# Optimization experiments

Measured on AMD Instinct MI355X. Metric: run time of the kernel, lower is better.

## Reference

```python
import jax, jax.numpy as jnp
import numpy as np

E = 8192       # number of edges
D = 256        # edge feature dim


def setup_inputs() -> dict:
    key = jax.random.key(0)
    ks = jax.random.split(key, 4)
    s = 1.0 / np.sqrt(D)
    return {
        "edge_x": jax.random.normal(ks[0], (E, D), dtype=jnp.float32),
        "W_sim1": jax.random.normal(ks[1], (D, D), dtype=jnp.float32) * s,
        "b_sim1": jnp.zeros((D,), dtype=jnp.float32),
        "W_sim2": jax.random.normal(ks[2], (D, D), dtype=jnp.float32) * s,
        "b_sim2": jnp.zeros((D,), dtype=jnp.float32),
        "W_out": jax.random.normal(ks[3], (3 * D, D), dtype=jnp.float32) * (1.0 / np.sqrt(3 * D)),
        "b_out": jnp.zeros((D,), dtype=jnp.float32),
    }


def reference(edge_x, W_sim1, b_sim1, W_sim2, b_sim2, W_out, b_out):
    # MPModule.forward, 'fully' branch.
    # LinearBlock = Linear + ReLU (assumed).
    e1 = jax.nn.relu(edge_x @ W_sim1 + b_sim1)            # [E, D]
    # (e1.unsqueeze(1) * e1).mean(-1)  ==  (e1 @ e1.T) / D, avoiding [E,E,D]
    sim1 = (e1 @ e1.T) / D                                 # [E, E]
    e2 = jax.nn.relu(edge_x @ W_sim2 + b_sim2)             # [E, D]
    sim2 = (e2 @ e2.T) / D                                 # [E, E]
    # (edge_x * sim.unsqueeze(-1)).sum(1) == sim @ edge_x
    agg1 = sim1 @ edge_x                                   # [E, D]
    agg2 = sim2 @ edge_x                                   # [E, D]
    h = jnp.concatenate([edge_x, agg1, agg2], axis=-1)     # [E, 3D]
    return jax.nn.relu(h @ W_out + b_out)                  # [E, D]
```

## Files before the change

kernel.cpp:

```cpp
#include <hip/hip_runtime.h>
#include <hip/hip_bf16.h>


typedef short bf16x8  __attribute__((ext_vector_type(8)));
typedef short short4v __attribute__((ext_vector_type(4)));
typedef float f32x4   __attribute__((ext_vector_type(4)));

__device__ inline short f2bf(float x) {
    unsigned u = __builtin_bit_cast(unsigned, x);
    return (short)((u + 0x7fffu + ((u >> 16) & 1u)) >> 16);
}
__device__ inline float bf2f(short b) {
    return __builtin_bit_cast(float, (unsigned)((unsigned short)b) << 16);
}
__device__ inline void cp16_async(const char* g, char* l) {
    __builtin_amdgcn_global_load_lds(
        (const __attribute__((address_space(1))) unsigned int*)g,
        (__attribute__((address_space(3))) unsigned int*)l, 16, 0, 0);
}

__device__ __forceinline__ void core128(
    const short* __restrict__ Ap, int lda, const short* __restrict__ Bp, int ldb,
    int kbeg, int kend, int m0, int n0, short* Sf, f32x4 acc[4][4], int t)
{
    const int l = t & 63, lr = l & 15, q = l >> 4;
    const int w = t >> 6, wm = w >> 1, wn = w & 1;
    const int wub = t & ~63;

    auto stage = [&](int buf, int k0) {
        #pragma unroll
        for (int it = 0; it < 4; ++it) {
            int idx = it * 256 + t, r = idx >> 3, s = idx & 7;
            cp16_async((const char*)(Ap + (size_t)(m0 + r) * lda + k0) + s * 16,
                       (char*)(Sf + buf * 16384) + (size_t)(it * 256 + wub) * 16);
        }
        #pragma unroll
        for (int it = 0; it < 4; ++it) {
            int idx = it * 256 + t, r = idx >> 3, s = idx & 7;
            cp16_async((const char*)(Bp + (size_t)(n0 + r) * ldb + k0) + s * 16,
                       (char*)(Sf + buf * 16384 + 8192) + (size_t)(it * 256 + wub) * 16);
        }
    };

    stage(0, kbeg);
    __syncthreads();
    int cur = 0;
    for (int k0 = kbeg; k0 < kend; k0 += 64) {
        if (k0 + 64 < kend) stage(cur ^ 1, k0 + 64);
        const short* As = Sf + cur * 16384;
        const short* Bs = As + 8192;
        #pragma unroll
        for (int ks = 0; ks < 2; ++ks) {
            bf16x8 af[4], bfr[4];
            #pragma unroll
            for (int mt = 0; mt < 4; ++mt) {
                int ar = wm * 64 + mt * 16 + lr;
                af[mt] = *(const bf16x8*)&As[ar * 64 + (((ks*4 + q) ^ (ar & 7)) << 3)];
            }
            #pragma unroll
            for (int nt = 0; nt < 4; ++nt) {
                int br = wn * 64 + nt * 16 + lr;
                bfr[nt] = *(const bf16x8*)&Bs[br * 64 + (((ks*4 + q) ^ (br & 7)) << 3)];
            }
            #pragma unroll
            for (int mt = 0; mt < 4; ++mt)
                #pragma unroll
                for (int nt = 0; nt < 4; ++nt)
                    acc[mt][nt] = __builtin_amdgcn_mfma_f32_16x16x32_bf16(
                        af[mt], bfr[nt], acc[mt][nt], 0, 0, 0);
        }
        __syncthreads();
        cur ^= 1;
    }
}

__global__ __launch_bounds__(256, 1)
void d1_eg(const float* __restrict__ X,
           const float* __restrict__ W1, const float* __restrict__ b1v,
           const float* __restrict__ W2, const float* __restrict__ b2v,
           const float* __restrict__ Wo,
           short* __restrict__ h, short* __restrict__ e1t, short* __restrict__ e2t,
           short* __restrict__ G1t, short* __restrict__ G2t,
           short* __restrict__ Bt4, int* __restrict__ ticket)
{
    const int bx = blockIdx.x, by = blockIdx.y, z = blockIdx.z;
    const int t = threadIdx.x;
    const int l = t & 63, lr = l & 15, q = l >> 4;
    const int w = t >> 6, wm = w >> 1, wn = w & 1;

    if (bx == 0 && by == 0 && z == 0 && t == 0) { ticket[0] = 0; ticket[1] = 0; }

    __shared__ __attribute__((aligned(16))) short S[32768];

    if (z == 2 && by == 0) {
        short (*tile)[33] = (short(*)[33])S;
        const int tx = t & 31, ty = t >> 5;
        const int kx = bx >> 3, ny = bx & 7;
        const int dk0 = kx * 32, k0l = kx * 32, n0l = ny * 32;
        #pragma unroll
        for (int i = 0; i < 4; ++i) {
            int row = ty + i * 8;
            tile[row][tx] = f2bf(Wo[(size_t)(k0l + row) * 256 + n0l + tx]);
        }
        __syncthreads();
        #pragma unroll
        for (int i = 0; i < 4; ++i) {
            int row = ty + i * 8;
            int n = n0l + row;
            int slot = ((((dk0 & 32) + tx) >> 3) ^ (n & 7));
            Bt4[(size_t)n * 768 + (dk0 & ~63) + slot * 8 + (tx & 7)] = tile[tx][row];
        }
        __syncthreads();
    }

    const float* Wz   = (z == 0) ? W1 : (z == 1) ? W2 : (Wo + (size_t)(z - 1) * 65536);
    const float* bias = (z == 0) ? b1v : (z == 1) ? b2v : nullptr;
    short* et         = (z == 0) ? e1t : (z == 1) ? e2t : (z == 2) ? G1t : G2t;
    const int  mode   = (z < 2) ? 1 : 3;
    const int  sim    = z & 1;
    const bool writeX = (z == 0 && by == 0);
    const int m0 = bx * 128, n0 = by * 128;

    f32x4 acc[4][4];
    #pragma unroll
    for (int i = 0; i < 4; ++i)
        #pragma unroll
        for (int j = 0; j < 4; ++j) acc[i][j] = f32x4{0.f, 0.f, 0.f, 0.f};

    f32x4 ra[4][2];
    float rb[4][8];

    auto loadAB = [&](int k0) {
        #pragma unroll
        for (int i = 0; i < 4; ++i) {
            int idx = i * 256 + t, r = idx >> 3, g = idx & 7;
            const float* xp = X + (size_t)(m0 + r) * 256 + k0 + g * 8;
            ra[i][0] = *(const f32x4*)xp;
            ra[i][1] = *(const f32x4*)(xp + 4);
        }
        #pragma unroll
        for (int i = 0; i < 4; ++i) {
            int idx = i * 256 + t, n = idx & 127, g = idx >> 7;
            const float* wp = Wz + (size_t)(k0 + g * 8) * 256 + n0 + n;
            #pragma unroll
            for (int j = 0; j < 8; ++j) rb[i][j] = wp[(size_t)j * 256];
        }
    };
    auto writeAB = [&](int buf, int k0) {
        #pragma unroll
        for (int i = 0; i < 4; ++i) {
            int idx = i * 256 + t, r = idx >> 3, g = idx & 7;
            bf16x8 pk;
            pk[0] = f2bf(ra[i][0][0]); pk[1] = f2bf(ra[i][0][1]);
            pk[2] = f2bf(ra[i][0][2]); pk[3] = f2bf(ra[i][0][3]);
            pk[4] = f2bf(ra[i][1][0]); pk[5] = f2bf(ra[i][1][1]);
            pk[6] = f2bf(ra[i][1][2]); pk[7] = f2bf(ra[i][1][3]);
            *(bf16x8*)&S[buf * 16384 + r * 64 + ((g ^ (r & 7)) << 3)] = pk;
            if (writeX)
                *(bf16x8*)(h + (size_t)(m0 + r) * 768 + k0 + ((g ^ (r & 7)) << 3)) = pk;
        }
        #pragma unroll
        for (int i = 0; i < 4; ++i) {
            int idx = i * 256 + t, n = idx & 127, g = idx >> 7;
            bf16x8 pk;
            #pragma unroll
            for (int j = 0; j < 8; ++j) pk[j] = f2bf(rb[i][j]);
            *(bf16x8*)&S[buf * 16384 + 8192 + n * 64 + ((g ^ (n & 7)) << 3)] = pk;
        }
    };

    loadAB(0);
    writeAB(0, 0);
    __syncthreads();
    int cur = 0;
    for (int k0 = 0; k0 < 256; k0 += 64) {
        const bool nx = (k0 + 64 < 256);
        if (nx) loadAB(k0 + 64);
        const short* As = S + cur * 16384;
        const short* Bs = As + 8192;
        #pragma unroll
        for (int ks = 0; ks < 2; ++ks) {
            bf16x8 af[4], bfr[4];
            #pragma unroll
            for (int mt = 0; mt < 4; ++mt) {
                int ar = wm * 64 + mt * 16 + lr;
                af[mt] = *(const bf16x8*)&As[ar * 64 + (((ks*4 + q) ^ (ar & 7)) << 3)];
            }
            #pragma unroll
            for (int nt = 0; nt < 4; ++nt) {
                int br = wn * 64 + nt * 16 + lr;
                bfr[nt] = *(const bf16x8*)&Bs[br * 64 + (((ks*4 + q) ^ (br & 7)) << 3)];
            }
            #pragma unroll
            for (int mt = 0; mt < 4; ++mt)
                #pragma unroll
                for (int nt = 0; nt < 4; ++nt)
                    acc[mt][nt] = __builtin_amdgcn_mfma_f32_16x16x32_bf16(
                        af[mt], bfr[nt], acc[mt][nt], 0, 0, 0);
        }
        if (nx) writeAB(cur ^ 1, k0 + 64);
        __syncthreads();
        cur ^= 1;
    }

    short* Hs = S;
    short* Ts = S + 16384;
    #pragma unroll
    for (int mt = 0; mt < 4; ++mt)
        #pragma unroll
        for (int nt = 0; nt < 4; ++nt) {
            int n_loc = wn * 64 + nt * 16 + lr;
            float bb = (mode == 1) ? bias[n0 + n_loc] : 0.f;
            short vb[4];
            #pragma unroll
            for (int r = 0; r < 4; ++r) {
                float v = acc[mt][nt][r] + bb;
                if (mode == 1) v = v > 0.f ? v : 0.f;
                vb[r] = f2bf(v);
                if (mode == 1) {
                    int m_loc = wm * 64 + mt * 16 + q * 4 + r;
                    Hs[m_loc * 128 + n_loc] = vb[r];
                }
            }
            int gm = wm * 8 + mt * 2 + (q >> 1);
            short4v pk = { vb[0], vb[1], vb[2], vb[3] };
            *(short4v*)&Ts[n_loc * 128 + ((gm >> 3) << 6)
                           + (((gm & 7) ^ (n_loc & 7)) << 3) + ((q & 1) << 2)] = pk;
        }
    __syncthreads();
    if (mode == 1) {
        const int cb = 256 + sim * 256 + n0;
        for (int i = t; i < 2048; i += 256) {
            int ml = i >> 4, g = i & 15;
            bf16x8 hv = *(const bf16x8*)&Hs[ml * 128 + g * 8];
            *(bf16x8*)(h + (size_t)(m0 + ml) * 768 + cb + ((g >> 3) << 6)
                       + (((g & 7) ^ (ml & 7)) << 3)) = hv;
        }
    }
    for (int i = t; i < 2048; i += 256) {
        int nl = i >> 4, s = i & 15;
        bf16x8 tv = *(const bf16x8*)&Ts[nl * 128 + s * 8];
        *(bf16x8*)(et + (size_t)(n0 + nl) * 8192 + m0 + s * 8) = tv;
    }
}

__global__ __launch_bounds__(256, 1)
void d23(const short* __restrict__ e1t, const short* __restrict__ e2t,
         const short* __restrict__ G1t, const short* __restrict__ G2t,
         const short* __restrict__ h, short* __restrict__ Bt4,
         float* __restrict__ Nslab, int* __restrict__ ticket,
         const float* __restrict__ bov, float* __restrict__ outf)
{
    const int fb = blockIdx.x, t = threadIdx.x;
    const int l = t & 63, lr = l & 15, q = l >> 4;
    const int w = t >> 6, wm = w >> 1, wn = w & 1;

    __shared__ __attribute__((aligned(16))) short S[32768];

    {
        const int bx = fb & 1, by = (fb >> 1) & 1, bz = fb >> 2;
        const int sim = bz & 1, split = bz >> 1;
        const int kbeg = split * 512, m0 = bx * 128, n0 = by * 128;
        const short* Ap = sim ? G2t : G1t;
        const short* Bp = sim ? e2t : e1t;

        f32x4 acc[4][4];
        #pragma unroll
        for (int i = 0; i < 4; ++i)
            #pragma unroll
            for (int j = 0; j < 4; ++j) acc[i][j] = f32x4{0.f, 0.f, 0.f, 0.f};
        core128(Ap, 8192, Bp, 8192, kbeg, kbeg + 512, m0, n0, S, acc, t);

        float* Mo = Nslab + (size_t)(split * 2 + sim) * 65536;
        #pragma unroll
        for (int mt = 0; mt < 4; ++mt)
            #pragma unroll
            for (int nt = 0; nt < 4; ++nt)
                #pragma unroll
                for (int r = 0; r < 4; ++r) {
                    int m = m0 + wm * 64 + mt * 16 + q * 4 + r;
                    int n = n0 + wn * 64 + nt * 16 + lr;
                    Mo[(size_t)m * 256 + n] = acc[mt][nt][r] * (1.0f / 256.0f);
                }
    }

    __syncthreads();
    if (t == 0) {
        __threadfence();
        __hip_atomic_fetch_add(&ticket[0], 1, __ATOMIC_ACQ_REL, __HIP_MEMORY_SCOPE_AGENT);
        while (__hip_atomic_load(&ticket[0], __ATOMIC_ACQUIRE, __HIP_MEMORY_SCOPE_AGENT) < 128)
            __builtin_amdgcn_s_sleep(8);
    }
    __syncthreads();
    __threadfence();

    if (t < 128) {
        int gid = fb * 128 + t;
        int simg = gid >> 13, rem = gid & 8191;
        int n = rem >> 5, g = rem & 31;
        f32x4 sa = f32x4{0.f, 0.f, 0.f, 0.f}, sb = f32x4{0.f, 0.f, 0.f, 0.f};
        #pragma unroll
        for (int s = 0; s < 16; ++s) {
            const float* np = Nslab + (size_t)(s * 2 + simg) * 65536
                              + (size_t)n * 256 + g * 8;
            sa += *(const f32x4*)np;
            sb += *(const f32x4*)(np + 4);
        }
        bf16x8 pk;
        pk[0] = f2bf(sa[0]); pk[1] = f2bf(sa[1]);
        pk[2] = f2bf(sa[2]); pk[3] = f2bf(sa[3]);
        pk[4] = f2bf(sb[0]); pk[5] = f2bf(sb[1]);
        pk[6] = f2bf(sb[2]); pk[7] = f2bf(sb[3]);
        int k = 256 + simg * 256 + g * 8;
        int slot = (g & 7) ^ (n & 7);
        *(bf16x8*)(Bt4 + (size_t)n * 768 + (k & ~63) + slot * 8) = pk;
    }

    __syncthreads();
    if (t == 0) {
        __threadfence();
        __hip_atomic_fetch_add(&ticket[1], 1, __ATOMIC_ACQ_REL, __HIP_MEMORY_SCOPE_AGENT);
        while (__hip_atomic_load(&ticket[1], __ATOMIC_ACQUIRE, __HIP_MEMORY_SCOPE_AGENT) < 128)
            __builtin_amdgcn_s_sleep(8);
    }
    __syncthreads();
    __threadfence();

    {
        const int m0 = (fb >> 1) * 128, n0 = (fb & 1) * 128;
        f32x4 acc[4][4];
        #pragma unroll
        for (int i = 0; i < 4; ++i)
            #pragma unroll
            for (int j = 0; j < 4; ++j) acc[i][j] = f32x4{0.f, 0.f, 0.f, 0.f};
        core128(h, 768, Bt4, 768, 0, 768, m0, n0, S, acc, t);

        #pragma unroll
        for (int mt = 0; mt < 4; ++mt)
            #pragma unroll
            for (int nt = 0; nt < 4; ++nt)
                #pragma unroll
                for (int r = 0; r < 4; ++r) {
                    int m = m0 + wm * 64 + mt * 16 + q * 4 + r;
                    int n = n0 + wn * 64 + nt * 16 + lr;
                    float v = acc[mt][nt][r] + bov[n];
                    outf[(size_t)m * 256 + n] = v > 0.f ? v : 0.f;
                }
    }
}

extern "C" void kernel_launch(void* const* d_in, const int* in_sizes, int n_in,
                              void* d_out, int out_size, void* d_ws, size_t ws_size,
                              hipStream_t stream)
{
    const float* edge_x = (const float*)d_in[0];
    const float* W1 = (const float*)d_in[1];
    const float* b1 = (const float*)d_in[2];
    const float* W2 = (const float*)d_in[3];
    const float* b2 = (const float*)d_in[4];
    const float* Wo = (const float*)d_in[5];
    const float* bo = (const float*)d_in[6];

    char* ws = (char*)d_ws;
    short* h     = (short*)ws;
    short* e1t   = (short*)(ws + 12582912);
    short* e2t   = (short*)(ws + 16777216);
    short* G1t   = (short*)(ws + 20971520);
    short* G2t   = (short*)(ws + 25165824);
    short* Bt4   = (short*)(ws + 29360128);
    float* Nslab = (float*)(ws + 29753344);
    int*   tick  = (int*)(ws + 38141952);

    float* out = (float*)d_out;

    d1_eg<<<dim3(64, 2, 4), 256, 0, stream>>>(
        edge_x, W1, b1, W2, b2, Wo, h, e1t, e2t, G1t, G2t, Bt4, tick);

    d23<<<dim3(128), 256, 0, stream>>>(
        e1t, e2t, G1t, G2t, h, Bt4, Nslab, tick, bo, out);
}
```

Measured before the change: 140.6 us.

## Split bf16 prep into its own kernel and double split-K grid to 256 blocks

Adds a prep kernel that converts X and all weights to pre-transposed, swizzled bf16 once, so the first GEMM kernel can use the shared async-copy core128 path instead of converting fp32 in registers on every block. The fused second kernel grows from 128 to 256 blocks: split-K depth halves, the reduction uses 32 slabs, and the final output GEMM uses 64-row tiles with its own async-staged loop. Barrier fences are relaxed to release/acquire atomics. The cost is an extra kernel launch, a larger Nslab workspace, and a persistent grid barrier that now needs all 256 blocks resident at once.

```diff
diff --git a/kernel.cpp b/kernel.cpp
--- a/kernel.cpp
+++ b/kernel.cpp
@@ -74,52 +74,79 @@
     }
 }
 
+__global__ void prep_all(const float* __restrict__ X, short* __restrict__ h,
+                         const float* __restrict__ W1, const float* __restrict__ W2,
+                         const float* __restrict__ Wo,
+                         short* __restrict__ Wt1, short* __restrict__ Wt2,
+                         short* __restrict__ Wto1, short* __restrict__ Wto2,
+                         short* __restrict__ Bt4, int* __restrict__ tick)
+{
+    __shared__ short tile[32][33];
+    const int tx = threadIdx.x, ty = threadIdx.y;
+    if (blockIdx.y < 8) {
+        const int r0 = blockIdx.x * 32, c0 = blockIdx.y * 32;
+        #pragma unroll
+        for (int i = 0; i < 4; ++i) {
+            int row = ty + i * 8;
+            short b = f2bf(X[(size_t)(r0 + row) * 256 + c0 + tx]);
+            int slot = ((((c0 & 32) + tx) >> 3) ^ ((r0 + row) & 7));
+            h[(size_t)(r0 + row) * 768 + (c0 & ~63) + slot * 8 + (tx & 7)] = b;
+        }
+        return;
+    }
+    int tw = (blockIdx.y - 8) * 256 + blockIdx.x;
+    if (tw >= 320) {
+        if (tw == 320 && tx == 0 && ty == 0) { tick[0] = 0; tick[1] = 0; }
+        return;
+    }
+    const float* src; short* dst; int ldwt, dk0, kx, ny;
+    if (tw < 64)       { src = W1; dst = Wt1; ldwt = 256;
+                         kx = tw >> 3; ny = tw & 7; dk0 = kx * 32; }
+    else if (tw < 128) { int u = tw - 64; src = W2; dst = Wt2; ldwt = 256;
+                         kx = u >> 3; ny = u & 7; dk0 = kx * 32; }
+    else               { int u = tw - 128; int g = u >> 6; int rem = u & 63;
+                         kx = rem >> 3; ny = rem & 7;
+                         src = Wo + (size_t)g * 65536;
+                         if (g == 0) { dst = Bt4; ldwt = 768; dk0 = kx * 32; }
+                         else        { dst = (g == 1) ? Wto1 : Wto2;
+                                       ldwt = 256; dk0 = kx * 32; } }
+    const int k0l = kx * 32, n0 = ny * 32;
+    #pragma unroll
+    for (int i = 0; i < 4; ++i) {
+        int row = ty + i * 8;
+        tile[row][tx] = f2bf(src[(size_t)(k0l + row) * 256 + n0 + tx]);
+    }
+    __syncthreads();
+    #pragma unroll
+    for (int i = 0; i < 4; ++i) {
+        int row = ty + i * 8;
+        int n = n0 + row;
+        int slot = ((((dk0 & 32) + tx) >> 3) ^ (n & 7));
+        dst[(size_t)n * ldwt + (dk0 & ~63) + slot * 8 + (tx & 7)] = tile[tx][row];
+    }
+}
+
 __global__ __launch_bounds__(256, 1)
-void d1_eg(const float* __restrict__ X,
-           const float* __restrict__ W1, const float* __restrict__ b1v,
-           const float* __restrict__ W2, const float* __restrict__ b2v,
-           const float* __restrict__ Wo,
-           short* __restrict__ h, short* __restrict__ e1t, short* __restrict__ e2t,
-           short* __restrict__ G1t, short* __restrict__ G2t,
-           short* __restrict__ Bt4, int* __restrict__ ticket)
-{
-    const int bx = blockIdx.x, by = blockIdx.y, z = blockIdx.z;
+void eg_gemm(short* __restrict__ h,
+             const short* __restrict__ Wt1, const short* __restrict__ Wt2,
+             const short* __restrict__ Wto1, const short* __restrict__ Wto2,
+             const float* __restrict__ b1, const float* __restrict__ b2,
+             short* __restrict__ e1t, short* __restrict__ e2t,
+             short* __restrict__ G1t, short* __restrict__ G2t)
+{
+    const int z = blockIdx.z;
+    const int mode = (z < 2) ? 1 : 3;
+    const int sim  = z & 1;
+    const short* Bp   = (z == 0) ? Wt1 : (z == 1) ? Wt2 : (z == 2) ? Wto1 : Wto2;
+    const float* bias = (z == 0) ? b1  : (z == 1) ? b2  : nullptr;
+    short* et         = (z == 0) ? e1t : (z == 1) ? e2t : (z == 2) ? G1t : G2t;
+
+    const int m0 = blockIdx.x * 128, n0 = blockIdx.y * 128;
     const int t = threadIdx.x;
     const int l = t & 63, lr = l & 15, q = l >> 4;
     const int w = t >> 6, wm = w >> 1, wn = w & 1;
 
-    if (bx == 0 && by == 0 && z == 0 && t == 0) { ticket[0] = 0; ticket[1] = 0; }
-
     __shared__ __attribute__((aligned(16))) short S[32768];
-
-    if (z == 2 && by == 0) {
-        short (*tile)[33] = (short(*)[33])S;
-        const int tx = t & 31, ty = t >> 5;
-        const int kx = bx >> 3, ny = bx & 7;
-        const int dk0 = kx * 32, k0l = kx * 32, n0l = ny * 32;
-        #pragma unroll
-        for (int i = 0; i < 4; ++i) {
-            int row = ty + i * 8;
-            tile[row][tx] = f2bf(Wo[(size_t)(k0l + row) * 256 + n0l + tx]);
-        }
-        __syncthreads();
-        #pragma unroll
-        for (int i = 0; i < 4; ++i) {
-            int row = ty + i * 8;
-            int n = n0l + row;
-            int slot = ((((dk0 & 32) + tx) >> 3) ^ (n & 7));
-            Bt4[(size_t)n * 768 + (dk0 & ~63) + slot * 8 + (tx & 7)] = tile[tx][row];
-        }
-        __syncthreads();
-    }
-
-    const float* Wz   = (z == 0) ? W1 : (z == 1) ? W2 : (Wo + (size_t)(z - 1) * 65536);
-    const float* bias = (z == 0) ? b1v : (z == 1) ? b2v : nullptr;
-    short* et         = (z == 0) ? e1t : (z == 1) ? e2t : (z == 2) ? G1t : G2t;
-    const int  mode   = (z < 2) ? 1 : 3;
-    const int  sim    = z & 1;
-    const bool writeX = (z == 0 && by == 0);
-    const int m0 = bx * 128, n0 = by * 128;
 
     f32x4 acc[4][4];
     #pragma unroll
@@ -127,81 +154,7 @@
         #pragma unroll
         for (int j = 0; j < 4; ++j) acc[i][j] = f32x4{0.f, 0.f, 0.f, 0.f};
 
-    f32x4 ra[4][2];
-    float rb[4][8];
-
-    auto loadAB = [&](int k0) {
-        #pragma unroll
-        for (int i = 0; i < 4; ++i) {
-            int idx = i * 256 + t, r = idx >> 3, g = idx & 7;
-            const float* xp = X + (size_t)(m0 + r) * 256 + k0 + g * 8;
-            ra[i][0] = *(const f32x4*)xp;
-            ra[i][1] = *(const f32x4*)(xp + 4);
-        }
-        #pragma unroll
-        for (int i = 0; i < 4; ++i) {
-            int idx = i * 256 + t, n = idx & 127, g = idx >> 7;
-            const float* wp = Wz + (size_t)(k0 + g * 8) * 256 + n0 + n;
-            #pragma unroll
-            for (int j = 0; j < 8; ++j) rb[i][j] = wp[(size_t)j * 256];
-        }
-    };
-    auto writeAB = [&](int buf, int k0) {
-        #pragma unroll
-        for (int i = 0; i < 4; ++i) {
-            int idx = i * 256 + t, r = idx >> 3, g = idx & 7;
-            bf16x8 pk;
-            pk[0] = f2bf(ra[i][0][0]); pk[1] = f2bf(ra[i][0][1]);
-            pk[2] = f2bf(ra[i][0][2]); pk[3] = f2bf(ra[i][0][3]);
-            pk[4] = f2bf(ra[i][1][0]); pk[5] = f2bf(ra[i][1][1]);
-            pk[6] = f2bf(ra[i][1][2]); pk[7] = f2bf(ra[i][1][3]);
-            *(bf16x8*)&S[buf * 16384 + r * 64 + ((g ^ (r & 7)) << 3)] = pk;
-            if (writeX)
-                *(bf16x8*)(h + (size_t)(m0 + r) * 768 + k0 + ((g ^ (r & 7)) << 3)) = pk;
-        }
-        #pragma unroll
-        for (int i = 0; i < 4; ++i) {
-            int idx = i * 256 + t, n = idx & 127, g = idx >> 7;
-            bf16x8 pk;
-            #pragma unroll
-            for (int j = 0; j < 8; ++j) pk[j] = f2bf(rb[i][j]);
-            *(bf16x8*)&S[buf * 16384 + 8192 + n * 64 + ((g ^ (n & 7)) << 3)] = pk;
-        }
-    };
-
-    loadAB(0);
-    writeAB(0, 0);
-    __syncthreads();
-    int cur = 0;
-    for (int k0 = 0; k0 < 256; k0 += 64) {
-        const bool nx = (k0 + 64 < 256);
-        if (nx) loadAB(k0 + 64);
-        const short* As = S + cur * 16384;
-        const short* Bs = As + 8192;
-        #pragma unroll
-        for (int ks = 0; ks < 2; ++ks) {
-            bf16x8 af[4], bfr[4];
-            #pragma unroll
-            for (int mt = 0; mt < 4; ++mt) {
-                int ar = wm * 64 + mt * 16 + lr;
-                af[mt] = *(const bf16x8*)&As[ar * 64 + (((ks*4 + q) ^ (ar & 7)) << 3)];
-            }
-            #pragma unroll
-            for (int nt = 0; nt < 4; ++nt) {
-                int br = wn * 64 + nt * 16 + lr;
-                bfr[nt] = *(const bf16x8*)&Bs[br * 64 + (((ks*4 + q) ^ (br & 7)) << 3)];
-            }
-            #pragma unroll
-            for (int mt = 0; mt < 4; ++mt)
-                #pragma unroll
-                for (int nt = 0; nt < 4; ++nt)
-                    acc[mt][nt] = __builtin_amdgcn_mfma_f32_16x16x32_bf16(
-                        af[mt], bfr[nt], acc[mt][nt], 0, 0, 0);
-        }
-        if (nx) writeAB(cur ^ 1, k0 + 64);
-        __syncthreads();
-        cur ^= 1;
-    }
+    core128(h, 768, Bp, 256, 0, 256, m0, n0, S, acc, t);
 
     short* Hs = S;
     short* Ts = S + 16384;
@@ -245,22 +198,22 @@
 }
 
 __global__ __launch_bounds__(256, 1)
-void d23(const short* __restrict__ e1t, const short* __restrict__ e2t,
-         const short* __restrict__ G1t, const short* __restrict__ G2t,
-         const short* __restrict__ h, short* __restrict__ Bt4,
-         float* __restrict__ Nslab, int* __restrict__ ticket,
-         const float* __restrict__ bov, float* __restrict__ outf)
+void d23v2(const short* __restrict__ e1t, const short* __restrict__ e2t,
+           const short* __restrict__ G1t, const short* __restrict__ G2t,
+           const short* __restrict__ h, short* __restrict__ Bt4,
+           float* __restrict__ Nslab, int* __restrict__ ticket,
+           const float* __restrict__ bov, float* __restrict__ outf)
 {
     const int fb = blockIdx.x, t = threadIdx.x;
     const int l = t & 63, lr = l & 15, q = l >> 4;
-    const int w = t >> 6, wm = w >> 1, wn = w & 1;
+    const int w = t >> 6, wm = w >> 1, wn = w & 1, wub = t & ~63;
 
     __shared__ __attribute__((aligned(16))) short S[32768];
 
     {
         const int bx = fb & 1, by = (fb >> 1) & 1, bz = fb >> 2;
         const int sim = bz & 1, split = bz >> 1;
-        const int kbeg = split * 512, m0 = bx * 128, n0 = by * 128;
+        const int kbeg = split * 256, m0 = bx * 128, n0 = by * 128;
         const short* Ap = sim ? G2t : G1t;
         const short* Bp = sim ? e2t : e1t;
 
@@ -269,7 +222,7 @@
         for (int i = 0; i < 4; ++i)
             #pragma unroll
             for (int j = 0; j < 4; ++j) acc[i][j] = f32x4{0.f, 0.f, 0.f, 0.f};
-        core128(Ap, 8192, Bp, 8192, kbeg, kbeg + 512, m0, n0, S, acc, t);
+        core128(Ap, 8192, Bp, 8192, kbeg, kbeg + 256, m0, n0, S, acc, t);
 
         float* Mo = Nslab + (size_t)(split * 2 + sim) * 65536;
         #pragma unroll
@@ -286,21 +239,19 @@
 
     __syncthreads();
     if (t == 0) {
-        __threadfence();
-        __hip_atomic_fetch_add(&ticket[0], 1, __ATOMIC_ACQ_REL, __HIP_MEMORY_SCOPE_AGENT);
-        while (__hip_atomic_load(&ticket[0], __ATOMIC_ACQUIRE, __HIP_MEMORY_SCOPE_AGENT) < 128)
+        __hip_atomic_fetch_add(&ticket[0], 1, __ATOMIC_RELEASE, __HIP_MEMORY_SCOPE_AGENT);
+        while (__hip_atomic_load(&ticket[0], __ATOMIC_ACQUIRE, __HIP_MEMORY_SCOPE_AGENT) < 256)
             __builtin_amdgcn_s_sleep(8);
     }
     __syncthreads();
-    __threadfence();
-
-    if (t < 128) {
-        int gid = fb * 128 + t;
+
+    if (t < 64) {
+        int gid = fb * 64 + t;
         int simg = gid >> 13, rem = gid & 8191;
         int n = rem >> 5, g = rem & 31;
         f32x4 sa = f32x4{0.f, 0.f, 0.f, 0.f}, sb = f32x4{0.f, 0.f, 0.f, 0.f};
-        #pragma unroll
-        for (int s = 0; s < 16; ++s) {
+        #pragma unroll 4
+        for (int s = 0; s < 32; ++s) {
             const float* np = Nslab + (size_t)(s * 2 + simg) * 65536
                               + (size_t)n * 256 + g * 8;
             sa += *(const f32x4*)np;
@@ -318,30 +269,73 @@
 
     __syncthreads();
     if (t == 0) {
-        __threadfence();
-        __hip_atomic_fetch_add(&ticket[1], 1, __ATOMIC_ACQ_REL, __HIP_MEMORY_SCOPE_AGENT);
-        while (__hip_atomic_load(&ticket[1], __ATOMIC_ACQUIRE, __HIP_MEMORY_SCOPE_AGENT) < 128)
+        __hip_atomic_fetch_add(&ticket[1], 1, __ATOMIC_RELEASE, __HIP_MEMORY_SCOPE_AGENT);
+        while (__hip_atomic_load(&ticket[1], __ATOMIC_ACQUIRE, __HIP_MEMORY_SCOPE_AGENT) < 256)
             __builtin_amdgcn_s_sleep(8);
     }
     __syncthreads();
-    __threadfence();
 
     {
-        const int m0 = (fb >> 1) * 128, n0 = (fb & 1) * 128;
-        f32x4 acc[4][4];
-        #pragma unroll
-        for (int i = 0; i < 4; ++i)
+        const int m0 = (fb >> 1) * 64, n0 = (fb & 1) * 128;
+        f32x4 acc[2][4];
+        #pragma unroll
+        for (int i = 0; i < 2; ++i)
             #pragma unroll
             for (int j = 0; j < 4; ++j) acc[i][j] = f32x4{0.f, 0.f, 0.f, 0.f};
-        core128(h, 768, Bt4, 768, 0, 768, m0, n0, S, acc, t);
-
-        #pragma unroll
-        for (int mt = 0; mt < 4; ++mt)
+
+        auto stage = [&](int buf, int k0) {
+            #pragma unroll
+            for (int it = 0; it < 2; ++it) {
+                int idx = it * 256 + t, r = idx >> 3, s = idx & 7;
+                cp16_async((const char*)(h + (size_t)(m0 + r) * 768 + k0) + s * 16,
+                           (char*)(S + buf * 12288) + (size_t)(it * 256 + wub) * 16);
+            }
+            #pragma unroll
+            for (int it = 0; it < 4; ++it) {
+                int idx = it * 256 + t, r = idx >> 3, s = idx & 7;
+                cp16_async((const char*)(Bt4 + (size_t)(n0 + r) * 768 + k0) + s * 16,
+                           (char*)(S + buf * 12288 + 4096) + (size_t)(it * 256 + wub) * 16);
+            }
+        };
+
+        stage(0, 0);
+        __syncthreads();
+        int cur = 0;
+        for (int k0 = 0; k0 < 768; k0 += 64) {
+            if (k0 + 64 < 768) stage(cur ^ 1, k0 + 64);
+            const short* As = S + cur * 12288;
+            const short* Bs = As + 4096;
+            #pragma unroll
+            for (int ks = 0; ks < 2; ++ks) {
+                bf16x8 af[2], bfr[4];
+                #pragma unroll
+                for (int mt = 0; mt < 2; ++mt) {
+                    int ar = wm * 32 + mt * 16 + lr;
+                    af[mt] = *(const bf16x8*)&As[ar * 64 + (((ks*4 + q) ^ (ar & 7)) << 3)];
+                }
+                #pragma unroll
+                for (int nt = 0; nt < 4; ++nt) {
+                    int br = wn * 64 + nt * 16 + lr;
+                    bfr[nt] = *(const bf16x8*)&Bs[br * 64 + (((ks*4 + q) ^ (br & 7)) << 3)];
+                }
+                #pragma unroll
+                for (int mt = 0; mt < 2; ++mt)
+                    #pragma unroll
+                    for (int nt = 0; nt < 4; ++nt)
+                        acc[mt][nt] = __builtin_amdgcn_mfma_f32_16x16x32_bf16(
+                            af[mt], bfr[nt], acc[mt][nt], 0, 0, 0);
+            }
+            __syncthreads();
+            cur ^= 1;
+        }
+
+        #pragma unroll
+        for (int mt = 0; mt < 2; ++mt)
             #pragma unroll
             for (int nt = 0; nt < 4; ++nt)
                 #pragma unroll
                 for (int r = 0; r < 4; ++r) {
-                    int m = m0 + wm * 64 + mt * 16 + q * 4 + r;
+                    int m = m0 + wm * 32 + mt * 16 + q * 4 + r;
                     int n = n0 + wn * 64 + nt * 16 + lr;
                     float v = acc[mt][nt][r] + bov[n];
                     outf[(size_t)m * 256 + n] = v > 0.f ? v : 0.f;
@@ -367,15 +361,22 @@
     short* e2t   = (short*)(ws + 16777216);
     short* G1t   = (short*)(ws + 20971520);
     short* G2t   = (short*)(ws + 25165824);
-    short* Bt4   = (short*)(ws + 29360128);
-    float* Nslab = (float*)(ws + 29753344);
-    int*   tick  = (int*)(ws + 38141952);
+    short* Wt1   = (short*)(ws + 29360128);
+    short* Wt2   = (short*)(ws + 29491200);
+    short* Wto1  = (short*)(ws + 29622272);
+    short* Wto2  = (short*)(ws + 29753344);
+    short* Bt4   = (short*)(ws + 29884416);
+    float* Nslab = (float*)(ws + 30277632);
+    int*   tick  = (int*)(ws + 47054848);
 
     float* out = (float*)d_out;
 
-    d1_eg<<<dim3(64, 2, 4), 256, 0, stream>>>(
-        edge_x, W1, b1, W2, b2, Wo, h, e1t, e2t, G1t, G2t, Bt4, tick);
-
-    d23<<<dim3(128), 256, 0, stream>>>(
+    prep_all<<<dim3(256, 10), dim3(32, 8), 0, stream>>>(
+        edge_x, h, W1, W2, Wo, Wt1, Wt2, Wto1, Wto2, Bt4, tick);
+
+    eg_gemm<<<dim3(64, 2, 4), 256, 0, stream>>>(
+        h, Wt1, Wt2, Wto1, Wto2, b1, b2, e1t, e2t, G1t, G2t);
+
+    d23v2<<<dim3(256), 256, 0, stream>>>(
         e1t, e2t, G1t, G2t, h, Bt4, Nslab, tick, bo, out);
 }
```

New measurement: 151.3 us. +7.6%, slower.
